# Kernel tuning notes

Measured on AMD Instinct MI355X. Metric: run time of the kernel, lower is better.

Reference implementation:

```python
import jax, jax.numpy as jnp
import numpy as np

H = 8          # num_heads
EPS = 1e-5     # nn.LayerNorm default eps


def _attn(x, kv, wq, bq, wk, bk, wv, bv, wo, bo):
    # x: [B, Nq, D] queries; kv: [B, Nk, D] keys/values. softmax over keys (dim=-1).
    B, Nq, D = x.shape
    Nk = kv.shape[1]
    d = D // H
    q = (x @ wq + bq).reshape(B, Nq, H, d).transpose(0, 2, 1, 3)   # [B,h,Nq,d]
    k = (kv @ wk + bk).reshape(B, Nk, H, d).transpose(0, 2, 1, 3)  # [B,h,Nk,d]
    v = (kv @ wv + bv).reshape(B, Nk, H, d).transpose(0, 2, 1, 3)  # [B,h,Nk,d]
    scores = jnp.einsum('bhqd,bhkd->bhqk', q, k) * (d ** -0.5)
    a = jax.nn.softmax(scores, axis=-1)                            # softmax_dim='keys'
    ctx = jnp.einsum('bhqk,bhkd->bhqd', a, v)
    ctx = ctx.transpose(0, 2, 1, 3).reshape(B, Nq, D)
    return ctx @ wo + bo


def _ln(x, g, b):
    mu = jnp.mean(x, axis=-1, keepdims=True)
    var = jnp.var(x, axis=-1, keepdims=True)  # biased, matches torch LayerNorm
    return (x - mu) * jax.lax.rsqrt(var + EPS) * g + b


def setup_inputs() -> dict:
    key = jax.random.key(0)
    B, Nq, Nk, D = 2, 2048, 4096, 512
    Hid = 4 * D
    ks = jax.random.split(key, 32)
    s = 0.02
    r = lambda i, shp: jax.random.normal(ks[i], shp, dtype=jnp.float32) * s
    inp = {
        'x': jax.random.normal(ks[0], (B, Nq, D), dtype=jnp.float32),
        'cross': jax.random.normal(ks[1], (B, Nk, D), dtype=jnp.float32),
        # cross-attention projections (stored as [in, out])
        'ca_wq': r(2, (D, D)), 'ca_bq': jnp.zeros((D,), jnp.float32),
        'ca_wk': r(3, (D, D)), 'ca_bk': jnp.zeros((D,), jnp.float32),
        'ca_wv': r(4, (D, D)), 'ca_bv': jnp.zeros((D,), jnp.float32),
        'ca_wo': r(5, (D, D)), 'ca_bo': jnp.zeros((D,), jnp.float32),
        # self-attention projections
        'sa_wq': r(6, (D, D)), 'sa_bq': jnp.zeros((D,), jnp.float32),
        'sa_wk': r(7, (D, D)), 'sa_bk': jnp.zeros((D,), jnp.float32),
        'sa_wv': r(8, (D, D)), 'sa_bv': jnp.zeros((D,), jnp.float32),
        'sa_wo': r(9, (D, D)), 'sa_bo': jnp.zeros((D,), jnp.float32),
        # layer norms
        'ln1_g': jnp.ones((D,), jnp.float32), 'ln1_b': jnp.zeros((D,), jnp.float32),
        'ln2_g': jnp.ones((D,), jnp.float32), 'ln2_b': jnp.zeros((D,), jnp.float32),
        # MLP
        'mlp_w1': r(10, (D, Hid)), 'mlp_b1': jnp.zeros((Hid,), jnp.float32),
        'mlp_w2': r(11, (Hid, D)), 'mlp_b2': jnp.zeros((D,), jnp.float32),
    }
    return inp


def reference(x, cross,
              ca_wq, ca_bq, ca_wk, ca_bk, ca_wv, ca_bv, ca_wo, ca_bo,
              sa_wq, sa_bq, sa_wk, sa_bk, sa_wv, sa_bv, sa_wo, sa_bo,
              ln1_g, ln1_b, ln2_g, ln2_b,
              mlp_w1, mlp_b1, mlp_w2, mlp_b2):
    # a) cross-attention
    xc = _attn(x, cross, ca_wq, ca_bq, ca_wk, ca_bk, ca_wv, ca_bv, ca_wo, ca_bo)
    # b,c) LN then self-attention (Q=K=V=ln1(xc))
    xn = _ln(xc, ln1_g, ln1_b)
    xs = _attn(xn, xn, sa_wq, sa_bq, sa_wk, sa_bk, sa_wv, sa_bv, sa_wo, sa_bo)
    # d) residual
    y = xc + xs
    # e,f) LN + GELU MLP (torch GELU default = exact erf)
    h1 = jax.nn.gelu(_ln(y, ln2_g, ln2_b) @ mlp_w1 + mlp_b1, approximate=False)
    z = h1 @ mlp_w2 + mlp_b2
    # g) residual
    return y + z
```

## Files before the change

### kernel.cpp

```cpp
#include <hip/hip_runtime.h>
#include <math.h>

typedef _Float16 f16;
typedef __attribute__((ext_vector_type(8))) _Float16 f16x8;
typedef __attribute__((ext_vector_type(4))) _Float16 f16x4;
typedef __attribute__((ext_vector_type(4))) float f32x4;
typedef __attribute__((ext_vector_type(2))) __fp16 h16x2;

#define QSCALE 0.1803368801111204f

__device__ __forceinline__ void gl_lds16(const f16* g, f16* l) {
    __builtin_amdgcn_global_load_lds((const __attribute__((address_space(1))) void*)g,
                                     (__attribute__((address_space(3))) void*)l, 16, 0, 0);
}

struct PrepArgs {
    const float* ws[10]; f16* wd[10];
    const float* x; f16* xh;
    const float* cross; f16* ch;
};
__global__ __launch_bounds__(256)
void prep_all(PrepArgs p) {
    __shared__ float t[32][33];
    int bid = blockIdx.x, tid = threadIdx.x;
    if (bid < 4096) {
        const float* W; f16* Wt; int K, N, nx, ky;
        if (bid < 2048) {
            int wi = bid >> 8, tl = bid & 255;
            W = p.ws[wi]; Wt = p.wd[wi]; K = 512; N = 512; nx = tl & 15; ky = tl >> 4;
        } else if (bid < 3072) {
            int tl = bid - 2048;
            W = p.ws[8]; Wt = p.wd[8]; K = 512; N = 2048; nx = tl & 63; ky = tl >> 6;
        } else {
            int tl = bid - 3072;
            W = p.ws[9]; Wt = p.wd[9]; K = 2048; N = 512; nx = tl & 15; ky = tl >> 4;
        }
        int tx = tid & 31, ty = tid >> 5;
        int n0 = nx * 32, k0 = ky * 32;
#pragma unroll
        for (int i = 0; i < 4; i++)
            t[ty + i * 8][tx] = W[(size_t)(k0 + ty + i * 8) * N + n0 + tx];
        __syncthreads();
#pragma unroll
        for (int i = 0; i < 4; i++)
            Wt[(size_t)(n0 + ty + i * 8) * K + k0 + tx] = (f16)t[tx][ty + i * 8];
    } else {
        const float* X; f16* Y; size_t cb;
        if (bid < 6144) { X = p.x; Y = p.xh; cb = bid - 4096; }
        else            { X = p.cross; Y = p.ch; cb = bid - 6144; }
        size_t i = (cb * 256 + tid) * 4;
        f32x4 v = *(const f32x4*)(X + i);
        f16x4 o;
        o[0] = (f16)v[0]; o[1] = (f16)v[1]; o[2] = (f16)v[2]; o[3] = (f16)v[3];
        *(f16x4*)(Y + i) = o;
    }
}

__global__ __launch_bounds__(256)
void transpose_v(const f16* __restrict__ Vh, f16* __restrict__ Vt, int Nk) {
    __shared__ f16 t[64][72];
    int bh = blockIdx.y, k0 = blockIdx.x * 64;
    int tid = threadIdx.x;
    int kr = tid >> 2, dc = (tid & 3) * 16;
    const f16* src = Vh + ((size_t)bh * Nk + k0 + kr) * 64 + dc;
    f16x8 a = *(const f16x8*)src;
    f16x8 b = *(const f16x8*)(src + 8);
    *(f16x8*)&t[kr][dc] = a;
    *(f16x8*)&t[kr][dc + 8] = b;
    __syncthreads();
    int dr = tid >> 2, kc = (tid & 3) * 16;
    f16x8 o0, o1;
#pragma unroll
    for (int j = 0; j < 8; j++) { o0[j] = t[kc + j][dr]; o1[j] = t[kc + 8 + j][dr]; }
    f16* dst = Vt + ((size_t)bh * 64 + dr) * Nk + k0 + kc;
    *(f16x8*)dst = o0;
    *(f16x8*)(dst + 8) = o1;
}

__global__ __launch_bounds__(128)
void layernorm_f16(const float* __restrict__ X, const float* __restrict__ g,
                   const float* __restrict__ bta, f16* __restrict__ Y)
{
    __shared__ float red[4];
    int row = blockIdx.x;
    int tid = threadIdx.x;
    const float* x = X + (size_t)row * 512;
    f32x4 v = *(const f32x4*)(x + tid * 4);
    float s  = v[0] + v[1] + v[2] + v[3];
    float ss = v[0] * v[0] + v[1] * v[1] + v[2] * v[2] + v[3] * v[3];
#pragma unroll
    for (int m = 1; m < 64; m <<= 1) {
        s  += __shfl_xor(s, m, 64);
        ss += __shfl_xor(ss, m, 64);
    }
    int wave = tid >> 6, lane = tid & 63;
    if (lane == 0) { red[wave * 2] = s; red[wave * 2 + 1] = ss; }
    __syncthreads();
    s = red[0] + red[2]; ss = red[1] + red[3];
    float mu  = s * (1.0f / 512);
    float var = ss * (1.0f / 512) - mu * mu;
    float inv = rsqrtf(var + 1e-5f);
    f32x4 gv = *(const f32x4*)(g + tid * 4);
    f32x4 bv = *(const f32x4*)(bta + tid * 4);
    f16x4 o;
#pragma unroll
    for (int i = 0; i < 4; i++) o[i] = (f16)((v[i] - mu) * inv * gv[i] + bv[i]);
    *(f16x4*)(Y + (size_t)row * 512 + tid * 4) = o;
}

__global__ __launch_bounds__(256)
void gemm_f16(const f16* __restrict__ A, const f16* __restrict__ Wt,
              const float* __restrict__ b0, const float* __restrict__ b1,
              const float* __restrict__ b2, const float* __restrict__ res,
              float* __restrict__ Cf32, f16* __restrict__ C16,
              f16* __restrict__ hm0, f16* __restrict__ hm1, f16* __restrict__ hm2,
              int N, int K, int NBshift, int fused, int act, float s0)
{
    __shared__ __align__(16) f16 As[128 * 64];
    __shared__ __align__(16) f16 Bs[128 * 64];
    int tid = threadIdx.x, lane = tid & 63, wave = tid >> 6;
    int quad = lane >> 4, ln16 = lane & 15;
    int wm = wave >> 1, wn = wave & 1;
    int bm0 = blockIdx.y * 128, bn0 = blockIdx.x * 128;

    f32x4 acc[4][4];
#pragma unroll
    for (int i = 0; i < 4; i++)
#pragma unroll
        for (int j = 0; j < 4; j++) acc[i][j] = (f32x4){0.f, 0.f, 0.f, 0.f};

    const f16* ag[4]; const f16* bg[4]; f16* al[4]; f16* bl[4];
#pragma unroll
    for (int j = 0; j < 4; j++) {
        int L = tid + j * 256;
        int row = L >> 3, cc = (L & 7) ^ (row & 7);
        ag[j] = A  + (size_t)(bm0 + row) * K + cc * 8;
        bg[j] = Wt + (size_t)(bn0 + row) * K + cc * 8;
        al[j] = As + (size_t)L * 8;
        bl[j] = Bs + (size_t)L * 8;
    }
    int sw0 = (quad ^ (ln16 & 7)) * 8, sw1 = ((4 + quad) ^ (ln16 & 7)) * 8;

    for (int kt = 0; kt < K; kt += 64) {
        __syncthreads();
#pragma unroll
        for (int j = 0; j < 4; j++) gl_lds16(ag[j], al[j]);
#pragma unroll
        for (int j = 0; j < 4; j++) gl_lds16(bg[j], bl[j]);
        __syncthreads();
#pragma unroll
        for (int h = 0; h < 2; h++) {
            int sw = h ? sw1 : sw0;
            f16x8 af[4], bf[4];
#pragma unroll
            for (int mt = 0; mt < 4; mt++)
                af[mt] = *(const f16x8*)&As[(wm * 64 + mt * 16 + ln16) * 64 + sw];
#pragma unroll
            for (int nt = 0; nt < 4; nt++)
                bf[nt] = *(const f16x8*)&Bs[(wn * 64 + nt * 16 + ln16) * 64 + sw];
#pragma unroll
            for (int mt = 0; mt < 4; mt++)
#pragma unroll
                for (int nt = 0; nt < 4; nt++)
                    acc[mt][nt] = __builtin_amdgcn_mfma_f32_16x16x32_f16(af[mt], bf[nt], acc[mt][nt], 0, 0, 0);
        }
#pragma unroll
        for (int j = 0; j < 4; j++) { ag[j] += 64; bg[j] += 64; }
    }

    int NB = 1 << NBshift;
#pragma unroll
    for (int mt = 0; mt < 4; mt++) {
#pragma unroll
        for (int nt = 0; nt < 4; nt++) {
            int row = bm0 + wm * 64 + mt * 16 + quad * 4;
            int col = bn0 + wn * 64 + nt * 16 + ln16;
            float bv;
            if (fused) {
                int seg = col >> 9;
                const float* bp = seg == 0 ? b0 : (seg == 1 ? b1 : b2);
                bv = bp[col & 511];
            } else bv = b0[col];
#pragma unroll
            for (int i = 0; i < 4; i++) {
                int r = row + i;
                float v = acc[mt][nt][i] + bv;
                size_t idx = (size_t)r * N + col;
                if (res) v += res[idx];
                if (act) v = 0.5f * v * (1.0f + erff(v * 0.70710678118654752f));
                if (Cf32) Cf32[idx] = v;
                if (C16) C16[idx] = (f16)v;
                if (hm0) {
                    int seg = col >> 9;
                    f16* hp = seg == 0 ? hm0 : (seg == 1 ? hm1 : hm2);
                    float vv = seg == 0 ? v * s0 : v;
                    int hh = (col >> 6) & 7, d = col & 63;
                    int bt = r >> NBshift, rr = r & (NB - 1);
                    hp[(((size_t)bt * 8 + hh) * NB + rr) * 64 + d] = (f16)vv;
                }
            }
        }
    }
}

__global__ __launch_bounds__(256)
void gemm64(const f16* __restrict__ A, const f16* __restrict__ Wt,
            const float* __restrict__ bias, const float* __restrict__ res,
            float* __restrict__ Cf32, f16* __restrict__ hm0,
            int N, int K, int NBshift, float s0)
{
    __shared__ __align__(16) f16 As[2][64 * 64];
    __shared__ __align__(16) f16 Bs[2][64 * 64];
    int tid = threadIdx.x, lane = tid & 63, wave = tid >> 6;
    int quad = lane >> 4, ln16 = lane & 15;
    int wm = wave >> 1, wn = wave & 1;
    int bm0 = blockIdx.y * 64, bn0 = blockIdx.x * 64;

    f32x4 acc[2][2];
#pragma unroll
    for (int i = 0; i < 2; i++)
#pragma unroll
        for (int j = 0; j < 2; j++) acc[i][j] = (f32x4){0.f, 0.f, 0.f, 0.f};

    const f16* ag[2]; const f16* bg[2]; int Loff[2];
#pragma unroll
    for (int j = 0; j < 2; j++) {
        int L = tid + j * 256;
        int row = L >> 3, cc = (L & 7) ^ (row & 7);
        ag[j] = A  + (size_t)(bm0 + row) * K + cc * 8;
        bg[j] = Wt + (size_t)(bn0 + row) * K + cc * 8;
        Loff[j] = L * 8;
    }
    int sw0 = (quad ^ (ln16 & 7)) * 8, sw1 = ((4 + quad) ^ (ln16 & 7)) * 8;

#pragma unroll
    for (int j = 0; j < 2; j++) { gl_lds16(ag[j], &As[0][Loff[j]]); gl_lds16(bg[j], &Bs[0][Loff[j]]); }
#pragma unroll
    for (int j = 0; j < 2; j++) { ag[j] += 64; bg[j] += 64; }

    int cur = 0;
    for (int kt = 0; kt < K; kt += 64) {
        __syncthreads();
        if (kt + 64 < K) {
            int nxt = cur ^ 1;
#pragma unroll
            for (int j = 0; j < 2; j++) { gl_lds16(ag[j], &As[nxt][Loff[j]]); gl_lds16(bg[j], &Bs[nxt][Loff[j]]); }
#pragma unroll
            for (int j = 0; j < 2; j++) { ag[j] += 64; bg[j] += 64; }
        }
        const f16* Ac = As[cur]; const f16* Bc = Bs[cur];
#pragma unroll
        for (int h = 0; h < 2; h++) {
            int sw = h ? sw1 : sw0;
            f16x8 af[2], bf[2];
#pragma unroll
            for (int mt = 0; mt < 2; mt++)
                af[mt] = *(const f16x8*)&Ac[(wm * 32 + mt * 16 + ln16) * 64 + sw];
#pragma unroll
            for (int nt = 0; nt < 2; nt++)
                bf[nt] = *(const f16x8*)&Bc[(wn * 32 + nt * 16 + ln16) * 64 + sw];
#pragma unroll
            for (int mt = 0; mt < 2; mt++)
#pragma unroll
                for (int nt = 0; nt < 2; nt++)
                    acc[mt][nt] = __builtin_amdgcn_mfma_f32_16x16x32_f16(af[mt], bf[nt], acc[mt][nt], 0, 0, 0);
        }
        cur ^= 1;
    }

    int NB = 1 << NBshift;
#pragma unroll
    for (int mt = 0; mt < 2; mt++) {
#pragma unroll
        for (int nt = 0; nt < 2; nt++) {
            int row = bm0 + wm * 32 + mt * 16 + quad * 4;
            int col = bn0 + wn * 32 + nt * 16 + ln16;
            float bv = bias[col];
#pragma unroll
            for (int i = 0; i < 4; i++) {
                int r = row + i;
                float v = acc[mt][nt][i] + bv;
                size_t idx = (size_t)r * N + col;
                if (res) v += res[idx];
                if (Cf32) Cf32[idx] = v;
                if (hm0) {
                    int hh = (col >> 6) & 7, d = col & 63;
                    int bt = r >> NBshift, rr = r & (NB - 1);
                    hm0[(((size_t)bt * 8 + hh) * NB + rr) * 64 + d] = (f16)(v * s0);
                }
            }
        }
    }
}

__global__ __launch_bounds__(256, 3)
void attention_split(const f16* __restrict__ Qh, const f16* __restrict__ Kh,
                     const f16* __restrict__ Vt, f16* __restrict__ Op,
                     float* __restrict__ Lsum, int Nk)
{
    __shared__ __align__(16) f16 Kt[2][64 * 64];
    __shared__ __align__(16) f16 Vs[2][64 * 64];
    __shared__ __align__(16) f16 Ps[4 * 32 * 64];
    int z = blockIdx.z, b = z >> 2, sp = z & 3;
    int h = blockIdx.y, bh = b * 8 + h;
    int Nkh = Nk >> 2;
    int tid = threadIdx.x, lane = tid & 63, wave = tid >> 6;
    int quad = lane >> 4, ln16 = lane & 15, l7 = ln16 & 7;
    int qrow0 = blockIdx.x * 128 + wave * 32;

    f16x8 qf[2][2];
#pragma unroll
    for (int qh = 0; qh < 2; qh++)
#pragma unroll
        for (int dh = 0; dh < 2; dh++)
            qf[qh][dh] = *(const f16x8*)(Qh + ((size_t)bh * 2048 + qrow0 + qh * 16 + ln16) * 64
                                         + dh * 32 + quad * 8);
    f16x8 ones;
#pragma unroll
    for (int j = 0; j < 8; j++) ones[j] = (f16)1.0f;

    f32x4 oacc[2][4], aol[2];
#pragma unroll
    for (int qh = 0; qh < 2; qh++) {
        aol[qh] = (f32x4){0.f, 0.f, 0.f, 0.f};
#pragma unroll
        for (int dt = 0; dt < 4; dt++) oacc[qh][dt] = (f32x4){0.f, 0.f, 0.f, 0.f};
    }

    const f16* kb = Kh + ((size_t)bh * Nk + sp * Nkh) * 64;
    const f16* vb = Vt + (size_t)bh * 64 * Nk + sp * Nkh;

    const f16* kg[2]; const f16* vg[2]; int Loff[2];
#pragma unroll
    for (int j = 0; j < 2; j++) {
        int L = tid + j * 256;
        int row = L >> 3, cc = (L & 7) ^ (row & 7);
        kg[j] = kb + (size_t)row * 64 + cc * 8;
        vg[j] = vb + (size_t)row * Nk + cc * 8;
        Loff[j] = L * 8;
    }

    int koff[4][2], voff[4][2], poff_r[2][2];
#pragma unroll
    for (int nt = 0; nt < 4; nt++)
#pragma unroll
        for (int dh = 0; dh < 2; dh++)
            koff[nt][dh] = (nt * 16 + ln16) * 64 + ((dh * 4 + quad) ^ l7) * 8;
#pragma unroll
    for (int dt = 0; dt < 4; dt++)
#pragma unroll
        for (int c = 0; c < 2; c++)
            voff[dt][c] = (dt * 16 + ln16) * 64 + ((c * 4 + quad) ^ l7) * 8;
    int pbase = wave * 2048;
#pragma unroll
    for (int qh = 0; qh < 2; qh++)
#pragma unroll
        for (int c = 0; c < 2; c++)
            poff_r[qh][c] = pbase + (qh * 16 + ln16) * 64 + ((c * 4 + quad) ^ l7) * 8;
    int pw_half = (quad & 1) * 4;
    int pw_rowc = quad >> 1;

#pragma unroll
    for (int j = 0; j < 2; j++) { gl_lds16(kg[j], &Kt[0][Loff[j]]); gl_lds16(vg[j], &Vs[0][Loff[j]]); }
#pragma unroll
    for (int j = 0; j < 2; j++) { kg[j] += 64 * 64; vg[j] += 64; }

    int cur = 0;
    for (int kt = 0; kt < Nkh; kt += 64) {
        __syncthreads();
        if (kt + 64 < Nkh) {
            int nxt = cur ^ 1;
#pragma unroll
            for (int j = 0; j < 2; j++) { gl_lds16(kg[j], &Kt[nxt][Loff[j]]); gl_lds16(vg[j], &Vs[nxt][Loff[j]]); }
#pragma unroll
            for (int j = 0; j < 2; j++) { kg[j] += 64 * 64; vg[j] += 64; }
        }
        const f16* Ktc = Kt[cur]; const f16* Vsc = Vs[cur];

        {
            f16x8 kf[4][2];
#pragma unroll
            for (int nt = 0; nt < 4; nt++)
#pragma unroll
                for (int dh = 0; dh < 2; dh++)
                    kf[nt][dh] = *(const f16x8*)&Ktc[koff[nt][dh]];
#pragma unroll
            for (int qh = 0; qh < 2; qh++) {
                int prow = pbase + (qh * 16 + ln16) * 64;
#pragma unroll
                for (int nt = 0; nt < 4; nt++) {
                    f32x4 zz = (f32x4){0.f, 0.f, 0.f, 0.f};
                    zz = __builtin_amdgcn_mfma_f32_16x16x32_f16(kf[nt][0], qf[qh][0], zz, 0, 0, 0);
                    zz = __builtin_amdgcn_mfma_f32_16x16x32_f16(kf[nt][1], qf[qh][1], zz, 0, 0, 0);
                    float e0 = exp2f(zz[0]), e1 = exp2f(zz[1]);
                    float e2 = exp2f(zz[2]), e3 = exp2f(zz[3]);
                    h16x2 pa = __builtin_amdgcn_cvt_pkrtz(e0, e1);
                    h16x2 pb = __builtin_amdgcn_cvt_pkrtz(e2, e3);
                    union { h16x2 h[2]; f16x4 v; } u;
                    u.h[0] = pa; u.h[1] = pb;
                    *(f16x4*)&Ps[prow + ((nt * 2 + pw_rowc) ^ l7) * 8 + pw_half] = u.v;
                }
            }
        }
        {
            f16x8 vf[4][2];
#pragma unroll
            for (int dt = 0; dt < 4; dt++)
#pragma unroll
                for (int c = 0; c < 2; c++)
                    vf[dt][c] = *(const f16x8*)&Vsc[voff[dt][c]];
#pragma unroll
            for (int qh = 0; qh < 2; qh++) {
                f16x8 pf0 = *(const f16x8*)&Ps[poff_r[qh][0]];
                f16x8 pf1 = *(const f16x8*)&Ps[poff_r[qh][1]];
                aol[qh] = __builtin_amdgcn_mfma_f32_16x16x32_f16(ones, pf0, aol[qh], 0, 0, 0);
                aol[qh] = __builtin_amdgcn_mfma_f32_16x16x32_f16(ones, pf1, aol[qh], 0, 0, 0);
#pragma unroll
                for (int dt = 0; dt < 4; dt++) {
                    oacc[qh][dt] = __builtin_amdgcn_mfma_f32_16x16x32_f16(vf[dt][0], pf0, oacc[qh][dt], 0, 0, 0);
                    oacc[qh][dt] = __builtin_amdgcn_mfma_f32_16x16x32_f16(vf[dt][1], pf1, oacc[qh][dt], 0, 0, 0);
                }
            }
        }
        cur ^= 1;
    }

#pragma unroll
    for (int qh = 0; qh < 2; qh++) {
        size_t rowb = ((size_t)(sp * 16 + bh) * 2048 + qrow0 + qh * 16 + ln16) * 64;
#pragma unroll
        for (int dt = 0; dt < 4; dt++) {
            f16x4 o4;
#pragma unroll
            for (int i = 0; i < 4; i++) o4[i] = (f16)oacc[qh][dt][i];
            *(f16x4*)&Op[rowb + dt * 16 + quad * 4] = o4;
        }
        if (quad == 0)
            Lsum[(size_t)(sp * 16 + bh) * 2048 + qrow0 + qh * 16 + ln16] = aol[qh][0];
    }
}

__global__ __launch_bounds__(256)
void attn_combine(const f16* __restrict__ Op, const float* __restrict__ Lsum,
                  f16* __restrict__ O)
{
    int t = blockIdx.x * 256 + threadIdx.x;
    int d = t & 63;
    int q = (t >> 6) & 2047;
    int bh = t >> 17;
    int b = bh >> 3, h = bh & 7;
    float l = 0.f, val = 0.f;
#pragma unroll
    for (int s = 0; s < 4; s++) {
        l   += Lsum[(size_t)(s * 16 + bh) * 2048 + q];
        val += (float)Op[((size_t)(s * 16 + bh) * 2048 + q) * 64 + d];
    }
    O[((size_t)b * 2048 + q) * 512 + h * 64 + d] = (f16)(val / l);
}

extern "C" void kernel_launch(void* const* d_in, const int* in_sizes, int n_in,
                              void* d_out, int out_size, void* d_ws, size_t ws_size,
                              hipStream_t stream)
{
    (void)in_sizes; (void)n_in; (void)out_size; (void)ws_size;
    const float* x      = (const float*)d_in[0];
    const float* cross  = (const float*)d_in[1];
    const float* ca_wq  = (const float*)d_in[2];
    const float* ca_bq  = (const float*)d_in[3];
    const float* ca_wk  = (const float*)d_in[4];
    const float* ca_bk  = (const float*)d_in[5];
    const float* ca_wv  = (const float*)d_in[6];
    const float* ca_bv  = (const float*)d_in[7];
    const float* ca_wo  = (const float*)d_in[8];
    const float* ca_bo  = (const float*)d_in[9];
    const float* sa_wq  = (const float*)d_in[10];
    const float* sa_bq  = (const float*)d_in[11];
    const float* sa_wk  = (const float*)d_in[12];
    const float* sa_bk  = (const float*)d_in[13];
    const float* sa_wv  = (const float*)d_in[14];
    const float* sa_bv  = (const float*)d_in[15];
    const float* sa_wo  = (const float*)d_in[16];
    const float* sa_bo  = (const float*)d_in[17];
    const float* ln1_g  = (const float*)d_in[18];
    const float* ln1_b  = (const float*)d_in[19];
    const float* ln2_g  = (const float*)d_in[20];
    const float* ln2_b  = (const float*)d_in[21];
    const float* mlp_w1 = (const float*)d_in[22];
    const float* mlp_b1 = (const float*)d_in[23];
    const float* mlp_w2 = (const float*)d_in[24];
    const float* mlp_b2 = (const float*)d_in[25];
    float* out = (float*)d_out;

    float* XC = (float*)d_ws;
    float* Yb = XC + 2097152;
    f16* fb   = (f16*)(Yb + 2097152);
    f16* xh     = fb;
    f16* crossh = xh + 2097152;
    f16* xnh    = crossh + 4194304;
    f16* xn2h   = xnh + 2097152;
    f16* Qh     = xn2h + 2097152;
    f16* Kh     = Qh + 2097152;
    f16* Vh     = Kh + 4194304;
    f16* Vtb    = Vh + 4194304;
    f16* ctxh   = Vtb + 4194304;
    f16* h1h    = ctxh + 2097152;
    f16* t_caq  = h1h + 8388608;
    f16* t_cak  = t_caq + 262144;
    f16* t_cav  = t_cak + 262144;
    f16* t_cao  = t_cav + 262144;
    f16* t_saq  = t_cao + 262144;
    f16* t_sak  = t_saq + 262144;
    f16* t_sav  = t_sak + 262144;
    f16* t_sao  = t_sav + 262144;
    f16* t_w1   = t_sao + 262144;
    f16* t_w2   = t_w1 + 1048576;
    float* Lsum = (float*)(t_w2 + 1048576);

    PrepArgs pa;
    pa.ws[0] = ca_wq; pa.wd[0] = t_caq;
    pa.ws[1] = ca_wk; pa.wd[1] = t_cak;
    pa.ws[2] = ca_wv; pa.wd[2] = t_cav;
    pa.ws[3] = ca_wo; pa.wd[3] = t_cao;
    pa.ws[4] = sa_wq; pa.wd[4] = t_saq;
    pa.ws[5] = sa_wk; pa.wd[5] = t_sak;
    pa.ws[6] = sa_wv; pa.wd[6] = t_sav;
    pa.ws[7] = sa_wo; pa.wd[7] = t_sao;
    pa.ws[8] = mlp_w1; pa.wd[8] = t_w1;
    pa.ws[9] = mlp_w2; pa.wd[9] = t_w2;
    pa.x = x; pa.xh = xh; pa.cross = cross; pa.ch = crossh;
    prep_all<<<10240, 256, 0, stream>>>(pa);

    gemm64<<<dim3(8, 64), 256, 0, stream>>>(xh, t_caq, ca_bq, nullptr, nullptr, Qh,
                                            512, 512, 11, QSCALE);
    gemm_f16<<<dim3(8, 64), 256, 0, stream>>>(crossh, t_cak, ca_bk, ca_bv, nullptr, nullptr,
        nullptr, nullptr, Kh, Vh, nullptr, 1024, 512, 12, 1, 0, 1.0f);
    transpose_v<<<dim3(64, 16), 256, 0, stream>>>(Vh, Vtb, 4096);
    attention_split<<<dim3(16, 8, 8), 256, 0, stream>>>(Qh, Kh, Vtb, h1h, Lsum, 4096);
    attn_combine<<<8192, 256, 0, stream>>>(h1h, Lsum, ctxh);
    gemm64<<<dim3(8, 64), 256, 0, stream>>>(ctxh, t_cao, ca_bo, nullptr, XC, nullptr,
                                            512, 512, 11, 1.0f);
    layernorm_f16<<<4096, 128, 0, stream>>>(XC, ln1_g, ln1_b, xnh);
    gemm_f16<<<dim3(12, 32), 256, 0, stream>>>(xnh, t_saq, sa_bq, sa_bk, sa_bv, nullptr,
        nullptr, nullptr, Qh, Kh, Vh, 1536, 512, 11, 1, 0, QSCALE);
    transpose_v<<<dim3(32, 16), 256, 0, stream>>>(Vh, Vtb, 2048);
    attention_split<<<dim3(16, 8, 8), 256, 0, stream>>>(Qh, Kh, Vtb, h1h, Lsum, 2048);
    attn_combine<<<8192, 256, 0, stream>>>(h1h, Lsum, ctxh);
    gemm64<<<dim3(8, 64), 256, 0, stream>>>(ctxh, t_sao, sa_bo, XC, Yb, nullptr,
                                            512, 512, 11, 1.0f);
    layernorm_f16<<<4096, 128, 0, stream>>>(Yb, ln2_g, ln2_b, xn2h);
    gemm_f16<<<dim3(16, 32), 256, 0, stream>>>(xn2h, t_w1, mlp_b1, nullptr, nullptr, nullptr,
        nullptr, h1h, nullptr, nullptr, nullptr, 2048, 512, 11, 0, 1, 1.0f);
    gemm64<<<dim3(8, 64), 256, 0, stream>>>(h1h, t_w2, mlp_b2, Yb, out, nullptr,
                                            512, 2048, 11, 1.0f);
}
```

Measured before the change: 373.8 us.

## Use 512-thread attention blocks sharing single-buffered K/V tiles

The attention kernel now runs 8 waves per block, each covering 32 query rows, so one 64x64 K/V tile loaded into LDS serves 256 query rows instead of 128. This halves the K/V global traffic per query. The double-buffered prefetch is dropped in favour of a single buffer that is loaded and then synchronised before compute in every iteration. Loads are no longer overlapped with MFMA work, which may expose memory latency. The grid is halved, giving fewer blocks to spread across CUs.

```diff
diff --git a/kernel.cpp b/kernel.cpp
--- a/kernel.cpp
+++ b/kernel.cpp
@@ -293,20 +293,20 @@
     }
 }
 
-__global__ __launch_bounds__(256, 3)
+__global__ __launch_bounds__(512, 4)
 void attention_split(const f16* __restrict__ Qh, const f16* __restrict__ Kh,
                      const f16* __restrict__ Vt, f16* __restrict__ Op,
                      float* __restrict__ Lsum, int Nk)
 {
-    __shared__ __align__(16) f16 Kt[2][64 * 64];
-    __shared__ __align__(16) f16 Vs[2][64 * 64];
-    __shared__ __align__(16) f16 Ps[4 * 32 * 64];
+    __shared__ __align__(16) f16 Kt[64 * 64];
+    __shared__ __align__(16) f16 Vs[64 * 64];
+    __shared__ __align__(16) f16 Ps[8 * 32 * 64];
     int z = blockIdx.z, b = z >> 2, sp = z & 3;
     int h = blockIdx.y, bh = b * 8 + h;
     int Nkh = Nk >> 2;
     int tid = threadIdx.x, lane = tid & 63, wave = tid >> 6;
     int quad = lane >> 4, ln16 = lane & 15, l7 = ln16 & 7;
-    int qrow0 = blockIdx.x * 128 + wave * 32;
+    int qrow0 = blockIdx.x * 256 + wave * 32;
 
     f16x8 qf[2][2];
 #pragma unroll
@@ -330,14 +330,14 @@
     const f16* kb = Kh + ((size_t)bh * Nk + sp * Nkh) * 64;
     const f16* vb = Vt + (size_t)bh * 64 * Nk + sp * Nkh;
 
-    const f16* kg[2]; const f16* vg[2]; int Loff[2];
-#pragma unroll
-    for (int j = 0; j < 2; j++) {
-        int L = tid + j * 256;
+    const f16* kg; const f16* vg; f16* kl; f16* vl;
+    {
+        int L = tid;
         int row = L >> 3, cc = (L & 7) ^ (row & 7);
-        kg[j] = kb + (size_t)row * 64 + cc * 8;
-        vg[j] = vb + (size_t)row * Nk + cc * 8;
-        Loff[j] = L * 8;
+        kg = kb + (size_t)row * 64 + cc * 8;
+        vg = vb + (size_t)row * Nk + cc * 8;
+        kl = Kt + (size_t)L * 8;
+        vl = Vs + (size_t)L * 8;
     }
 
     int koff[4][2], voff[4][2], poff_r[2][2];
@@ -360,22 +360,12 @@
     int pw_half = (quad & 1) * 4;
     int pw_rowc = quad >> 1;
 
-#pragma unroll
-    for (int j = 0; j < 2; j++) { gl_lds16(kg[j], &Kt[0][Loff[j]]); gl_lds16(vg[j], &Vs[0][Loff[j]]); }
-#pragma unroll
-    for (int j = 0; j < 2; j++) { kg[j] += 64 * 64; vg[j] += 64; }
-
-    int cur = 0;
     for (int kt = 0; kt < Nkh; kt += 64) {
         __syncthreads();
-        if (kt + 64 < Nkh) {
-            int nxt = cur ^ 1;
-#pragma unroll
-            for (int j = 0; j < 2; j++) { gl_lds16(kg[j], &Kt[nxt][Loff[j]]); gl_lds16(vg[j], &Vs[nxt][Loff[j]]); }
-#pragma unroll
-            for (int j = 0; j < 2; j++) { kg[j] += 64 * 64; vg[j] += 64; }
-        }
-        const f16* Ktc = Kt[cur]; const f16* Vsc = Vs[cur];
+        gl_lds16(kg, kl);
+        gl_lds16(vg, vl);
+        __syncthreads();
+        kg += 64 * 64; vg += 64;
 
         {
             f16x8 kf[4][2];
@@ -383,7 +373,7 @@
             for (int nt = 0; nt < 4; nt++)
 #pragma unroll
                 for (int dh = 0; dh < 2; dh++)
-                    kf[nt][dh] = *(const f16x8*)&Ktc[koff[nt][dh]];
+                    kf[nt][dh] = *(const f16x8*)&Kt[koff[nt][dh]];
 #pragma unroll
             for (int qh = 0; qh < 2; qh++) {
                 int prow = pbase + (qh * 16 + ln16) * 64;
@@ -408,7 +398,7 @@
             for (int dt = 0; dt < 4; dt++)
 #pragma unroll
                 for (int c = 0; c < 2; c++)
-                    vf[dt][c] = *(const f16x8*)&Vsc[voff[dt][c]];
+                    vf[dt][c] = *(const f16x8*)&Vs[voff[dt][c]];
 #pragma unroll
             for (int qh = 0; qh < 2; qh++) {
                 f16x8 pf0 = *(const f16x8*)&Ps[poff_r[qh][0]];
@@ -422,7 +412,6 @@
                 }
             }
         }
-        cur ^= 1;
     }
 
 #pragma unroll
@@ -535,7 +524,7 @@
     gemm_f16<<<dim3(8, 64), 256, 0, stream>>>(crossh, t_cak, ca_bk, ca_bv, nullptr, nullptr,
         nullptr, nullptr, Kh, Vh, nullptr, 1024, 512, 12, 1, 0, 1.0f);
     transpose_v<<<dim3(64, 16), 256, 0, stream>>>(Vh, Vtb, 4096);
-    attention_split<<<dim3(16, 8, 8), 256, 0, stream>>>(Qh, Kh, Vtb, h1h, Lsum, 4096);
+    attention_split<<<dim3(8, 8, 8), 512, 0, stream>>>(Qh, Kh, Vtb, h1h, Lsum, 4096);
     attn_combine<<<8192, 256, 0, stream>>>(h1h, Lsum, ctxh);
     gemm64<<<dim3(8, 64), 256, 0, stream>>>(ctxh, t_cao, ca_bo, nullptr, XC, nullptr,
                                             512, 512, 11, 1.0f);
@@ -543,7 +532,7 @@
     gemm_f16<<<dim3(12, 32), 256, 0, stream>>>(xnh, t_saq, sa_bq, sa_bk, sa_bv, nullptr,
         nullptr, nullptr, Qh, Kh, Vh, 1536, 512, 11, 1, 0, QSCALE);
     transpose_v<<<dim3(32, 16), 256, 0, stream>>>(Vh, Vtb, 2048);
-    attention_split<<<dim3(16, 8, 8), 256, 0, stream>>>(Qh, Kh, Vtb, h1h, Lsum, 2048);
+    attention_split<<<dim3(8, 8, 8), 512, 0, stream>>>(Qh, Kh, Vtb, h1h, Lsum, 2048);
     attn_combine<<<8192, 256, 0, stream>>>(h1h, Lsum, ctxh);
     gemm64<<<dim3(8, 64), 256, 0, stream>>>(ctxh, t_sao, sa_bo, XC, Yb, nullptr,
                                             512, 512, 11, 1.0f);
```

After: 367.4 us. Within noise of the previous version (-1.7%).
